# Performance work log

Measured on AMD Instinct MI355X. Metric: run time of the kernel, lower is better.

## Reference

```python
import jax, jax.numpy as jnp
import numpy as np

B, N = 16, 512            # graphs, atoms per graph
F_DIM, H, D = 128, 64, 16  # feature_dim, hidden_dim, far_source_dim
CUT, GROWTH = 5.0, 2.0
NS, NT = 3, 2
MULT = GROWTH ** NS        # default far_max_radius_multiplier = 8
EMAX = CUT * MULT          # 40.0
TOT = NS + NT              # 5 shells total
SF = D + 3                 # 19 per-shell features
SE_IN = TOT * SF           # 95
EH_IN = 4 * D + SE_IN      # 159
N_RBF = 8
BOUNDS = [(5.0, 10.0), (10.0, 20.0), (20.0, 40.0), (40.0, 80.0), (80.0, float('inf'))]


def ln(x, g, b):
    m = x.mean(-1, keepdims=True)
    v = x.var(-1, keepdims=True)
    return (x - m) / jnp.sqrt(v + 1e-5) * g + b


def setup_inputs() -> dict:
    key = jax.random.key(0)
    ks = jax.random.split(key, 16)
    W = lambda k, i, o: jax.random.normal(k, (i, o), jnp.float32) / np.sqrt(i)
    inp = {}
    inp['x'] = jax.random.normal(ks[0], (B * N, F_DIM), jnp.float32)
    inp['pos'] = jax.random.uniform(ks[1], (B * N, 3), jnp.float32) * 80.0
    inp['batch'] = jnp.repeat(jnp.arange(B, dtype=jnp.int32), N)
    inp['num_graphs'] = B
    inp['in_ln_g'] = jnp.ones(F_DIM); inp['in_ln_b'] = jnp.zeros(F_DIM)
    inp['src_w1'] = W(ks[2], F_DIM, H); inp['src_b1'] = jnp.zeros(H)
    inp['src_w2'] = W(ks[3], H, D);     inp['src_b2'] = jnp.zeros(D)
    inp['src_ln_g'] = jnp.ones(D); inp['src_ln_b'] = jnp.zeros(D)
    inp['se_ln_g'] = jnp.ones(SE_IN); inp['se_ln_b'] = jnp.zeros(SE_IN)
    inp['se_w1'] = W(ks[4], SE_IN, H); inp['se_b1'] = jnp.zeros(H)
    inp['se_w2'] = W(ks[5], H, D);     inp['se_b2'] = jnp.zeros(D)
    inp['eh_ln_g'] = jnp.ones(EH_IN); inp['eh_ln_b'] = jnp.zeros(EH_IN)
    inp['eh_w1'] = W(ks[6], EH_IN, H); inp['eh_b1'] = jnp.zeros(H)
    inp['eh_w2'] = W(ks[7], H, 1);     inp['eh_b2'] = jnp.zeros(1)
    inp['k_screen'] = jnp.float32(-8.0)
    inp['kg_w1'] = W(ks[8], N_RBF + 2, 32); inp['kg_b1'] = jnp.zeros(32)
    inp['kg_w2'] = jnp.zeros((32, 1)); inp['kg_b2'] = jnp.zeros(1)  # zero-init per source
    inp['far_gate'] = jnp.float32(0.2)
    inp['energy_scale'] = jnp.float32(0.0)
    return inp


def reference(x, pos, batch, num_graphs, in_ln_g, in_ln_b, src_w1, src_b1, src_w2, src_b2,
              src_ln_g, src_ln_b, se_ln_g, se_ln_b, se_w1, se_b1, se_w2, se_b2,
              eh_ln_g, eh_ln_b, eh_w1, eh_b1, eh_w2, eh_b2,
              k_screen, kg_w1, kg_b1, kg_w2, kg_b2, far_gate, energy_scale):
    M = x.shape[0]
    n = M // num_graphs
    # per-atom source features
    h = ln(x, in_ln_g, in_ln_b)
    src = jax.nn.silu(h @ src_w1 + src_b1) @ src_w2 + src_b2
    src = ln(src, src_ln_g, src_ln_b)
    # graph-wise neutralization (subtract per-graph mean)
    gsum = jax.ops.segment_sum(src, batch, num_segments=num_graphs)
    cnt = jax.ops.segment_sum(jnp.ones((M, 1), x.dtype), batch, num_segments=num_graphs)
    src = src - (gsum / jnp.maximum(cnt, 1.0))[batch]
    # pairwise distances per graph
    p = pos.reshape(num_graphs, n, 3)
    s = src.reshape(num_graphs, n, D)
    diff = p[:, :, None, :] - p[:, None, :, :]
    d = jnp.sqrt((diff * diff).sum(-1) + 1e-12)  # [B,n,n]
    not_self = ~jnp.eye(n, dtype=bool)[None]
    # physical kernel with learned RBF gate
    screening = jax.nn.softplus(k_screen)
    base = jnp.exp(-screening * d) / jnp.maximum(d, 1e-6)
    centers = jnp.linspace(CUT, EMAX, N_RBF)
    spacing = (EMAX - CUT) / (N_RBF - 1)
    gamma = 1.0 / (spacing * spacing)
    dc = d[..., None]
    rbf = jnp.exp(-gamma * (dc - centers) ** 2)
    gin = jnp.concatenate([dc / CUT, dc / EMAX, rbf], -1)
    gate = 1.0 + jnp.tanh(jax.nn.silu(gin @ kg_w1 + kg_b1) @ kg_w2 + kg_b2)[..., 0]
    ker = base * gate
    # shell statistics: kernel-weighted mean source, count, mean_r, rms_r per shell
    feats = []
    for lo, up in BOUNDS:
        m = (d >= lo) & not_self
        if np.isfinite(up):
            m = m & (d < up)
        mf = m.astype(x.dtype)
        c = mf.sum(-1)
        denom = jnp.maximum(c, 1.0)
        mean = jnp.einsum('bij,bjc->bic', ker * mf, s) / denom[..., None]
        mr = (mf * d).sum(-1) / denom
        rr = jnp.sqrt((mf * d * d).sum(-1) / denom + 1e-12)
        feats.append(jnp.concatenate([mean, c[..., None], mr[..., None], rr[..., None]], -1))
    shell = jnp.concatenate(feats, -1).reshape(M, SE_IN)  # [M, 95]
    emb = jax.nn.silu(ln(shell, se_ln_g, se_ln_b) @ se_w1 + se_b1) @ se_w2 + se_b2
    ein = jnp.concatenate([src, emb, src * emb, src - emb, shell], -1)  # [M, 159]
    pa = (jax.nn.silu(ln(ein, eh_ln_g, eh_ln_b) @ eh_w1 + eh_b1) @ eh_w2 + eh_b2)[..., 0]
    pa = pa * jnp.tanh(far_gate) * jnp.exp(energy_scale)
    return jax.ops.segment_sum(pa, batch, num_segments=num_graphs)  # per-graph energies [B]
```

## Files before the change

### kernel.cpp

```cpp
#include <hip/hip_runtime.h>
#include <hip/hip_bf16.h>
#include <math.h>

#define B_G   16
#define N_A   512
#define M_AT  8192
#define FD    128
#define HD    64
#define DD    16
#define SEIN  95
#define EHIN  159
#define NLUT  512
#define DMAXF 140.0f

__device__ __forceinline__ float silu_f(float z) { return z / (1.f + __expf(-z)); }

__global__ __launch_bounds__(128) void k_front(
    const float* __restrict__ x,
    const float* __restrict__ g, const float* __restrict__ bb,
    const float* __restrict__ w1, const float* __restrict__ b1,
    const float* __restrict__ w2, const float* __restrict__ b2,
    const float* __restrict__ lng, const float* __restrict__ lnb,
    const float* __restrict__ k_screen,
    const float* __restrict__ kg_w1, const float* __restrict__ kg_b1,
    const float* __restrict__ kg_w2, const float* __restrict__ kg_b2,
    float* __restrict__ srcout, float* __restrict__ partials,
    float2* __restrict__ lut, float* __restrict__ out) {
  int t = threadIdx.x;

  if (blockIdx.x >= 256) {
    int lb = blockIdx.x - 256;
    __shared__ float w1l[320], b1l[32], w2l[32];
    if (lb == 0 && t < B_G) out[t] = 0.f;
    for (int idx = t; idx < 320; idx += 128) w1l[idx] = kg_w1[idx];
    if (t < 32) { b1l[t] = kg_b1[t]; w2l[t] = kg_w2[t]; }
    __syncthreads();
    int i = lb * 128 + t;
    float step = DMAXF / (float)(NLUT - 1);
    float ksv = k_screen[0];
    float screening = fmaxf(ksv, 0.f) + log1pf(expf(-fabsf(ksv)));
    float b2v = kg_b2[0];
    float vals[2];
#pragma unroll
    for (int e = 0; e < 2; ++e) {
      int ii = min(i + e, NLUT - 1);
      float d = (float)ii * step;
      float base = expf(-screening * d) / fmaxf(d, 1e-6f);
      float gin[10];
      gin[0] = d * (1.f / 5.0f);
      gin[1] = d * (1.f / 40.0f);
#pragma unroll
      for (int kk = 0; kk < 8; ++kk) {
        float u = d - (5.0f + 5.0f * (float)kk);
        gin[2 + kk] = expf(-(1.f / 25.f) * u * u);
      }
      float accv = 0.f;
      for (int h = 0; h < 32; ++h) {
        float z = b1l[h];
#pragma unroll
        for (int kk = 0; kk < 10; ++kk) z += gin[kk] * w1l[kk * 32 + h];
        accv += silu_f(z) * w2l[h];
      }
      vals[e] = base * (1.f + tanhf(accv + b2v));
    }
    lut[i] = make_float2(vals[0], vals[1] - vals[0]);
    return;
  }

  int wave = t >> 6, lane = t & 63;
  __shared__ __align__(16) float xnsA[2][FD][16];
  __shared__ __align__(16) float hbA[2][HD][16];
  __shared__ float psum[2][16];

  int aBase = blockIdx.x * 32 + wave * 16;
  int al = lane & 15, prt = lane >> 4;

  float xr[32];
  const float4* xp = (const float4*)(x + (size_t)(aBase + al) * FD + prt * 32);
#pragma unroll
  for (int i = 0; i < 8; ++i) {
    float4 v = xp[i];
    xr[i*4] = v.x; xr[i*4+1] = v.y; xr[i*4+2] = v.z; xr[i*4+3] = v.w;
  }
  float s = 0.f;
#pragma unroll
  for (int i = 0; i < 32; ++i) s += xr[i];
  s += __shfl_xor(s, 16); s += __shfl_xor(s, 32);
  float m = s * (1.f / 128.f);
  float v2 = 0.f;
#pragma unroll
  for (int i = 0; i < 32; ++i) { float d = xr[i] - m; v2 += d * d; }
  v2 += __shfl_xor(v2, 16); v2 += __shfl_xor(v2, 32);
  float inv = rsqrtf(v2 * (1.f / 128.f) + 1e-5f);
#pragma unroll
  for (int i = 0; i < 32; ++i) {
    int k = prt * 32 + i;
    xnsA[wave][k][al] = (xr[i] - m) * inv * g[k] + bb[k];
  }
  __syncthreads();

  int h0 = al * 4, a0 = prt * 4;
  float acc[4][4] = {};
#pragma unroll 4
  for (int k = 0; k < FD; ++k) {
    float4 wv = ((const float4*)(w1 + (size_t)k * HD))[al];
    float4 xa = *(const float4*)&xnsA[wave][k][a0];
    acc[0][0] += wv.x * xa.x; acc[0][1] += wv.x * xa.y; acc[0][2] += wv.x * xa.z; acc[0][3] += wv.x * xa.w;
    acc[1][0] += wv.y * xa.x; acc[1][1] += wv.y * xa.y; acc[1][2] += wv.y * xa.z; acc[1][3] += wv.y * xa.w;
    acc[2][0] += wv.z * xa.x; acc[2][1] += wv.z * xa.y; acc[2][2] += wv.z * xa.z; acc[2][3] += wv.z * xa.w;
    acc[3][0] += wv.w * xa.x; acc[3][1] += wv.w * xa.y; acc[3][2] += wv.w * xa.z; acc[3][3] += wv.w * xa.w;
  }
  {
    float4 bv = ((const float4*)b1)[al];
    float bh[4] = {bv.x, bv.y, bv.z, bv.w};
#pragma unroll
    for (int i = 0; i < 4; ++i) {
      float4 o;
      o.x = silu_f(acc[i][0] + bh[i]); o.y = silu_f(acc[i][1] + bh[i]);
      o.z = silu_f(acc[i][2] + bh[i]); o.w = silu_f(acc[i][3] + bh[i]);
      *(float4*)&hbA[wave][h0 + i][a0] = o;
    }
  }
  __syncthreads();

  float acc2[4] = {};
#pragma unroll 4
  for (int h = 0; h < HD; ++h) {
    float wv = w2[h * DD + al];
    float4 hv = *(const float4*)&hbA[wave][h][a0];
    acc2[0] += wv * hv.x; acc2[1] += wv * hv.y; acc2[2] += wv * hv.z; acc2[3] += wv * hv.w;
  }
  float b2c = b2[al], lgc = lng[al], lbc = lnb[al];
  float lsum = 0.f;
#pragma unroll
  for (int j = 0; j < 4; ++j) {
    float val = acc2[j] + b2c;
    float sm = val;
    sm += __shfl_xor(sm, 1); sm += __shfl_xor(sm, 2); sm += __shfl_xor(sm, 4); sm += __shfl_xor(sm, 8);
    float mm = sm * (1.f / 16.f);
    float dv = val - mm;
    float vv = dv * dv;
    vv += __shfl_xor(vv, 1); vv += __shfl_xor(vv, 2); vv += __shfl_xor(vv, 4); vv += __shfl_xor(vv, 8);
    float iv = rsqrtf(vv * (1.f / 16.f) + 1e-5f);
    float ov = dv * iv * lgc + lbc;
    srcout[(size_t)(aBase + a0 + j) * DD + al] = ov;
    lsum += ov;
  }
  lsum += __shfl_xor(lsum, 16); lsum += __shfl_xor(lsum, 32);
  if (lane < 16) psum[wave][al] = lsum;
  __syncthreads();
  if (t < 16) partials[(size_t)blockIdx.x * 16 + t] = psum[0][t] + psum[1][t];
}

__global__ __launch_bounds__(256) void k_pairs(
    const float* __restrict__ pos, const float* __restrict__ src,
    const float2* __restrict__ lut, const float* __restrict__ partials,
    float* __restrict__ shell) {
  int gph = blockIdx.x >> 7;
  int blk = blockIdx.x & 127;
  int t = threadIdx.x, wave = t >> 6, lane = t & 63;
  int i_local = blk * 4 + wave;

  __shared__ __align__(16) float sp[N_A * 3];
  __shared__ __align__(16) float ss[N_A * DD];
  __shared__ __align__(16) float2 luts[NLUT];
  __shared__ __align__(16) float wb[4][N_A];
  __shared__ unsigned char tbs[4][N_A];
  __shared__ float smean[16];

  for (int idx = t; idx < N_A * 3 / 4; idx += 256)
    ((float4*)sp)[idx] = ((const float4*)(pos + (size_t)gph * N_A * 3))[idx];
  for (int idx = t; idx < N_A * DD / 4; idx += 256)
    ((float4*)ss)[idx] = ((const float4*)(src + (size_t)gph * N_A * DD))[idx];
  if (t < NLUT / 2) ((float4*)luts)[t] = ((const float4*)lut)[t];
  if (t < 64) {
    int c = t & 15, grp = t >> 4;
    float sm = 0.f;
#pragma unroll
    for (int k = 0; k < 4; ++k)
      sm += partials[(size_t)(gph * 16 + grp * 4 + k) * 16 + c];
    sm += __shfl_xor(sm, 16); sm += __shfl_xor(sm, 32);
    if (t < 16) smean[c] = sm * (1.f / 512.f);
  }
  __syncthreads();

  float px = sp[i_local * 3], py = sp[i_local * 3 + 1], pz = sp[i_local * 3 + 2];
  float cnt[5] = {0,0,0,0,0}, sd[5] = {0,0,0,0,0}, sdd[5] = {0,0,0,0,0}, sw[5] = {0,0,0,0,0};
  const float lscale = (float)(NLUT - 1) / DMAXF;

#pragma unroll
  for (int it = 0; it < 8; ++it) {
    int jv = lane + it * 64;
    float dx = px - sp[jv * 3], dy = py - sp[jv * 3 + 1], dz = pz - sp[jv * 3 + 2];
    float d2 = dx * dx + dy * dy + dz * dz + 1e-12f;
    float d = sqrtf(d2);
    bool valid = (jv != i_local) && (d >= 5.0f);
    int tq = (d >= 10.f) + (d >= 20.f) + (d >= 40.f) + (d >= 80.f);
    float xq = d * lscale;
    int i0 = min((int)xq, NLUT - 2);
    float f = xq - (float)i0;
    float2 L = luts[i0];
    float w = valid ? (L.x + L.y * f) : 0.f;
    wb[wave][jv] = w;
    tbs[wave][jv] = (unsigned char)tq;
    float dm = valid ? d : 0.f;
    float ddm = valid ? d * d : 0.f;
    float cm = valid ? 1.f : 0.f;
#pragma unroll
    for (int q = 0; q < 5; ++q) {
      bool mq = (tq == q);
      cnt[q] += mq ? cm : 0.f;
      sd[q]  += mq ? dm : 0.f;
      sdd[q] += mq ? ddm : 0.f;
      sw[q]  += mq ? w : 0.f;
    }
  }
#pragma unroll
  for (int q = 0; q < 5; ++q) {
#pragma unroll
    for (int o = 32; o > 0; o >>= 1) {
      cnt[q] += __shfl_xor(cnt[q], o);
      sd[q]  += __shfl_xor(sd[q], o);
      sdd[q] += __shfl_xor(sdd[q], o);
      sw[q]  += __shfl_xor(sw[q], o);
    }
  }
  __syncthreads();

  int jlow = lane & 15, cq = lane >> 4;
  float accq[5][4] = {};
  const float* ssb = &ss[jlow * DD + cq * 4];
  const float* wbb = &wb[wave][jlow];
  const unsigned char* tbb = &tbs[wave][jlow];
#pragma unroll
  for (int jj = 0; jj < 32; ++jj) {
    float4 sv = *(const float4*)(ssb + jj * 256);
    float w = wbb[jj * 16];
    int tq = tbb[jj * 16];
    float w0 = (tq == 0) ? w : 0.f;
    float w1_ = (tq == 1) ? w : 0.f;
    float w2_ = (tq == 2) ? w : 0.f;
    float w3_ = (tq == 3) ? w : 0.f;
    float w4_ = (tq == 4) ? w : 0.f;
    accq[0][0] += w0 * sv.x; accq[0][1] += w0 * sv.y; accq[0][2] += w0 * sv.z; accq[0][3] += w0 * sv.w;
    accq[1][0] += w1_ * sv.x; accq[1][1] += w1_ * sv.y; accq[1][2] += w1_ * sv.z; accq[1][3] += w1_ * sv.w;
    accq[2][0] += w2_ * sv.x; accq[2][1] += w2_ * sv.y; accq[2][2] += w2_ * sv.z; accq[2][3] += w2_ * sv.w;
    accq[3][0] += w3_ * sv.x; accq[3][1] += w3_ * sv.y; accq[3][2] += w3_ * sv.z; accq[3][3] += w3_ * sv.w;
    accq[4][0] += w4_ * sv.x; accq[4][1] += w4_ * sv.y; accq[4][2] += w4_ * sv.z; accq[4][3] += w4_ * sv.w;
  }
#pragma unroll
  for (int q = 0; q < 5; ++q)
#pragma unroll
    for (int i = 0; i < 4; ++i) {
      float v = accq[q][i];
      v += __shfl_xor(v, 1); v += __shfl_xor(v, 2); v += __shfl_xor(v, 4); v += __shfl_xor(v, 8);
      accq[q][i] = v;
    }

  float* shp = shell + (size_t)(gph * N_A + i_local) * SEIN;
  if (jlow == 0) {
#pragma unroll
    for (int q = 0; q < 5; ++q) {
      float denom = fmaxf(cnt[q], 1.f);
#pragma unroll
      for (int i = 0; i < 4; ++i) {
        int c = cq * 4 + i;
        shp[q * 19 + c] = (accq[q][i] - smean[c] * sw[q]) / denom;
      }
    }
  }
  if (lane < 5) {
    int q = lane;
    float denom = fmaxf(cnt[q], 1.f);
    shp[q * 19 + 16] = cnt[q];
    shp[q * 19 + 17] = sd[q] / denom;
    shp[q * 19 + 18] = sqrtf(sdd[q] / denom + 1e-12f);
  }
}

__global__ __launch_bounds__(128) void k_tail(
    const float* __restrict__ src, const float* __restrict__ shell,
    const float* __restrict__ partials,
    const float* __restrict__ se_ln_g, const float* __restrict__ se_ln_b,
    const float* __restrict__ se_w1, const float* __restrict__ se_b1,
    const float* __restrict__ se_w2, const float* __restrict__ se_b2,
    const float* __restrict__ eh_ln_g, const float* __restrict__ eh_ln_b,
    const float* __restrict__ eh_w1, const float* __restrict__ eh_b1,
    const float* __restrict__ eh_w2, const float* __restrict__ eh_b2,
    const float* __restrict__ far_gate, const float* __restrict__ energy_scale,
    float* __restrict__ out) {
  int t = threadIdx.x, wave = t >> 6, lane = t & 63;
  __shared__ __align__(16) float einA[2][EHIN][16];
  __shared__ __align__(16) float shnA[2][SEIN][16];
  __shared__ __align__(16) float hbA[2][HD][16];
  __shared__ float smean[16];
  __shared__ float redv[2][4];

  int aB = blockIdx.x * 32;
  int gph = aB >> 9;

  if (t < 64) {
    int c = t & 15, grp = t >> 4;
    float sm = 0.f;
#pragma unroll
    for (int k = 0; k < 4; ++k)
      sm += partials[(size_t)(gph * 16 + grp * 4 + k) * 16 + c];
    sm += __shfl_xor(sm, 16); sm += __shfl_xor(sm, 32);
    if (t < 16) smean[c] = sm * (1.f / 512.f);
  }

  const float* shg = shell + (size_t)aB * SEIN;
  for (int idx = t; idx < 32 * SEIN; idx += 128) {
    unsigned a_loc = ((unsigned)idx * 690u) >> 16;
    int kk = idx - (int)a_loc * SEIN;
    einA[a_loc >> 4][64 + kk][a_loc & 15] = shg[idx];
  }
  __syncthreads();

  int al = lane & 15, prt = lane >> 4;
  {
    float s1 = 0.f, sq = 0.f;
    for (int i = 0; i < 24; ++i) {
      int k = prt * 24 + i;
      if (k < SEIN) { float v = einA[wave][64 + k][al]; s1 += v; sq += v * v; }
    }
    s1 += __shfl_xor(s1, 16); s1 += __shfl_xor(s1, 32);
    sq += __shfl_xor(sq, 16); sq += __shfl_xor(sq, 32);
    float m = s1 * (1.f / (float)SEIN);
    float var = sq * (1.f / (float)SEIN) - m * m;
    float inv = rsqrtf(var + 1e-5f);
    for (int i = 0; i < 24; ++i) {
      int k = prt * 24 + i;
      if (k < SEIN)
        shnA[wave][k][al] = (einA[wave][64 + k][al] - m) * inv * se_ln_g[k] + se_ln_b[k];
    }
  }
  __syncthreads();

  int h0 = al * 4, a0 = prt * 4;
  {
    float acc[4][4] = {};
#pragma unroll 5
    for (int k = 0; k < SEIN; ++k) {
      float4 wv = ((const float4*)(se_w1 + (size_t)k * HD))[al];
      float4 xa = *(const float4*)&shnA[wave][k][a0];
      acc[0][0] += wv.x * xa.x; acc[0][1] += wv.x * xa.y; acc[0][2] += wv.x * xa.z; acc[0][3] += wv.x * xa.w;
      acc[1][0] += wv.y * xa.x; acc[1][1] += wv.y * xa.y; acc[1][2] += wv.y * xa.z; acc[1][3] += wv.y * xa.w;
      acc[2][0] += wv.z * xa.x; acc[2][1] += wv.z * xa.y; acc[2][2] += wv.z * xa.z; acc[2][3] += wv.z * xa.w;
      acc[3][0] += wv.w * xa.x; acc[3][1] += wv.w * xa.y; acc[3][2] += wv.w * xa.z; acc[3][3] += wv.w * xa.w;
    }
    float4 bv = ((const float4*)se_b1)[al];
    float bh[4] = {bv.x, bv.y, bv.z, bv.w};
#pragma unroll
    for (int i = 0; i < 4; ++i) {
      float4 o;
      o.x = silu_f(acc[i][0] + bh[i]); o.y = silu_f(acc[i][1] + bh[i]);
      o.z = silu_f(acc[i][2] + bh[i]); o.w = silu_f(acc[i][3] + bh[i]);
      *(float4*)&hbA[wave][h0 + i][a0] = o;
    }
  }
  __syncthreads();

  {
    float acc2[4] = {};
#pragma unroll 4
    for (int h = 0; h < HD; ++h) {
      float wv = se_w2[h * DD + al];
      float4 hv = *(const float4*)&hbA[wave][h][a0];
      acc2[0] += wv * hv.x; acc2[1] += wv * hv.y; acc2[2] += wv * hv.z; acc2[3] += wv * hv.w;
    }
    float b2c = se_b2[al], smc = smean[al];
    int aW = aB + wave * 16;
#pragma unroll
    for (int j = 0; j < 4; ++j) {
      float ev = acc2[j] + b2c;
      float sv = src[(size_t)(aW + a0 + j) * DD + al] - smc;
      einA[wave][al][a0 + j] = sv;
      einA[wave][16 + al][a0 + j] = ev;
      einA[wave][32 + al][a0 + j] = sv * ev;
      einA[wave][48 + al][a0 + j] = sv - ev;
    }
  }
  __syncthreads();

  {
    float s1 = 0.f, sq = 0.f;
    for (int i = 0; i < 40; ++i) {
      int k = prt * 40 + i;
      if (k < EHIN) { float v = einA[wave][k][al]; s1 += v; sq += v * v; }
    }
    s1 += __shfl_xor(s1, 16); s1 += __shfl_xor(s1, 32);
    sq += __shfl_xor(sq, 16); sq += __shfl_xor(sq, 32);
    float m = s1 * (1.f / (float)EHIN);
    float var = sq * (1.f / (float)EHIN) - m * m;
    float inv = rsqrtf(var + 1e-5f);
    for (int i = 0; i < 40; ++i) {
      int k = prt * 40 + i;
      if (k < EHIN)
        einA[wave][k][al] = (einA[wave][k][al] - m) * inv * eh_ln_g[k] + eh_ln_b[k];
    }
  }
  __syncthreads();

  {
    float acc[4][4] = {};
#pragma unroll 3
    for (int k = 0; k < EHIN; ++k) {
      float4 wv = ((const float4*)(eh_w1 + (size_t)k * HD))[al];
      float4 xa = *(const float4*)&einA[wave][k][a0];
      acc[0][0] += wv.x * xa.x; acc[0][1] += wv.x * xa.y; acc[0][2] += wv.x * xa.z; acc[0][3] += wv.x * xa.w;
      acc[1][0] += wv.y * xa.x; acc[1][1] += wv.y * xa.y; acc[1][2] += wv.y * xa.z; acc[1][3] += wv.y * xa.w;
      acc[2][0] += wv.z * xa.x; acc[2][1] += wv.z * xa.y; acc[2][2] += wv.z * xa.z; acc[2][3] += wv.z * xa.w;
      acc[3][0] += wv.w * xa.x; acc[3][1] += wv.w * xa.y; acc[3][2] += wv.w * xa.z; acc[3][3] += wv.w * xa.w;
    }
    float4 b1v = ((const float4*)eh_b1)[al];
    float4 w2v = ((const float4*)eh_w2)[al];
    float bh[4] = {b1v.x, b1v.y, b1v.z, b1v.w};
    float wh[4] = {w2v.x, w2v.y, w2v.z, w2v.w};
    float pa[4] = {0.f, 0.f, 0.f, 0.f};
#pragma unroll
    for (int i = 0; i < 4; ++i)
#pragma unroll
      for (int j = 0; j < 4; ++j) pa[j] += silu_f(acc[i][j] + bh[i]) * wh[i];
#pragma unroll
    for (int j = 0; j < 4; ++j) {
      pa[j] += __shfl_xor(pa[j], 1); pa[j] += __shfl_xor(pa[j], 2);
      pa[j] += __shfl_xor(pa[j], 4); pa[j] += __shfl_xor(pa[j], 8);
    }
    if (al == 0) redv[wave][prt] = pa[0] + pa[1] + pa[2] + pa[3] + 4.f * eh_b2[0];
  }
  __syncthreads();
  if (t == 0) {
    float tot = 0.f;
#pragma unroll
    for (int w_ = 0; w_ < 2; ++w_)
#pragma unroll
      for (int p = 0; p < 4; ++p) tot += redv[w_][p];
    atomicAdd(&out[gph], tot * tanhf(far_gate[0]) * expf(energy_scale[0]));
  }
}

extern "C" void kernel_launch(void* const* d_in, const int* in_sizes, int n_in,
                              void* d_out, int out_size, void* d_ws, size_t ws_size,
                              hipStream_t stream) {
  const float* x         = (const float*)d_in[0];
  const float* pos       = (const float*)d_in[1];
  const float* in_ln_g   = (const float*)d_in[4];
  const float* in_ln_b   = (const float*)d_in[5];
  const float* src_w1    = (const float*)d_in[6];
  const float* src_b1    = (const float*)d_in[7];
  const float* src_w2    = (const float*)d_in[8];
  const float* src_b2    = (const float*)d_in[9];
  const float* src_ln_g  = (const float*)d_in[10];
  const float* src_ln_b  = (const float*)d_in[11];
  const float* se_ln_g   = (const float*)d_in[12];
  const float* se_ln_b   = (const float*)d_in[13];
  const float* se_w1     = (const float*)d_in[14];
  const float* se_b1     = (const float*)d_in[15];
  const float* se_w2     = (const float*)d_in[16];
  const float* se_b2     = (const float*)d_in[17];
  const float* eh_ln_g   = (const float*)d_in[18];
  const float* eh_ln_b   = (const float*)d_in[19];
  const float* eh_w1     = (const float*)d_in[20];
  const float* eh_b1     = (const float*)d_in[21];
  const float* eh_w2     = (const float*)d_in[22];
  const float* eh_b2     = (const float*)d_in[23];
  const float* k_screen  = (const float*)d_in[24];
  const float* kg_w1     = (const float*)d_in[25];
  const float* kg_b1     = (const float*)d_in[26];
  const float* kg_w2     = (const float*)d_in[27];
  const float* kg_b2     = (const float*)d_in[28];
  const float* far_gate  = (const float*)d_in[29];
  const float* en_scale  = (const float*)d_in[30];
  float* out = (float*)d_out;

  float* ws_src   = (float*)d_ws;
  float* ws_shell = ws_src + (size_t)M_AT * DD;
  float* ws_part  = ws_shell + (size_t)M_AT * SEIN;
  float2* ws_lut  = (float2*)(ws_part + 256 * 16);

  k_front<<<260, 128, 0, stream>>>(x, in_ln_g, in_ln_b, src_w1, src_b1,
                                   src_w2, src_b2, src_ln_g, src_ln_b,
                                   k_screen, kg_w1, kg_b1, kg_w2, kg_b2,
                                   ws_src, ws_part, ws_lut, out);
  k_pairs<<<B_G * (N_A / 4), 256, 0, stream>>>(pos, ws_src, ws_lut, ws_part, ws_shell);
  k_tail<<<M_AT / 32, 128, 0, stream>>>(ws_src, ws_shell, ws_part,
                                        se_ln_g, se_ln_b, se_w1, se_b1, se_w2, se_b2,
                                        eh_ln_g, eh_ln_b, eh_w1, eh_b1, eh_w2, eh_b2,
                                        far_gate, en_scale, out);
}
```

Before: 209.3 us.

## Remap front and tail MLPs to one atom per 16-lane group, more blocks

The front and tail MLP kernels previously gave each wave 16 atoms, with every lane computing a 4x4 hidden-by-atom tile. They now give each 16-lane group one atom, with each lane computing 4 hidden units, and use atom-major shared layouts padded to avoid bank conflicts. Blocks grow to 256 threads but cover 16 atoms, so the launch count doubles (512 blocks) to expose more parallelism across CUs. The trade-off is less register reuse of each weight load: every atom group now reads the full weight matrix itself, which adds global/L1 weight traffic.

```diff
diff --git a/kernel.cpp b/kernel.cpp
--- a/kernel.cpp
+++ b/kernel.cpp
@@ -1,5 +1,4 @@
 #include <hip/hip_runtime.h>
-#include <hip/hip_bf16.h>
 #include <math.h>
 
 #define B_G   16
@@ -12,10 +11,11 @@
 #define EHIN  159
 #define NLUT  512
 #define DMAXF 140.0f
+#define NFB   512
 
 __device__ __forceinline__ float silu_f(float z) { return z / (1.f + __expf(-z)); }
 
-__global__ __launch_bounds__(128) void k_front(
+__global__ __launch_bounds__(256) void k_front(
     const float* __restrict__ x,
     const float* __restrict__ g, const float* __restrict__ bb,
     const float* __restrict__ w1, const float* __restrict__ b1,
@@ -28,14 +28,14 @@
     float2* __restrict__ lut, float* __restrict__ out) {
   int t = threadIdx.x;
 
-  if (blockIdx.x >= 256) {
-    int lb = blockIdx.x - 256;
+  if (blockIdx.x >= NFB) {
+    int lb = blockIdx.x - NFB;
     __shared__ float w1l[320], b1l[32], w2l[32];
     if (lb == 0 && t < B_G) out[t] = 0.f;
-    for (int idx = t; idx < 320; idx += 128) w1l[idx] = kg_w1[idx];
+    for (int idx = t; idx < 320; idx += 256) w1l[idx] = kg_w1[idx];
     if (t < 32) { b1l[t] = kg_b1[t]; w2l[t] = kg_w2[t]; }
     __syncthreads();
-    int i = lb * 128 + t;
+    int i = lb * 256 + t;
     float step = DMAXF / (float)(NLUT - 1);
     float ksv = k_screen[0];
     float screening = fmaxf(ksv, 0.f) + log1pf(expf(-fabsf(ksv)));
@@ -68,73 +68,84 @@
   }
 
   int wave = t >> 6, lane = t & 63;
-  __shared__ __align__(16) float xnsA[2][FD][16];
-  __shared__ __align__(16) float hbA[2][HD][16];
-  __shared__ float psum[2][16];
-
-  int aBase = blockIdx.x * 32 + wave * 16;
-  int al = lane & 15, prt = lane >> 4;
-
-  float xr[32];
-  const float4* xp = (const float4*)(x + (size_t)(aBase + al) * FD + prt * 32);
-#pragma unroll
-  for (int i = 0; i < 8; ++i) {
-    float4 v = xp[i];
-    xr[i*4] = v.x; xr[i*4+1] = v.y; xr[i*4+2] = v.z; xr[i*4+3] = v.w;
+  int ag = lane >> 4, l16 = lane & 15;
+  int a = wave * 4 + ag;
+  int atom = blockIdx.x * 16 + a;
+
+  __shared__ __align__(16) float xn[16 * 132];
+  __shared__ __align__(16) float hb[16 * 68];
+  __shared__ float psum[4][16];
+
+  float xr[8];
+  {
+    const float4* xp = (const float4*)(x + (size_t)atom * FD + l16 * 8);
+    float4 v0 = xp[0], v1 = xp[1];
+    xr[0] = v0.x; xr[1] = v0.y; xr[2] = v0.z; xr[3] = v0.w;
+    xr[4] = v1.x; xr[5] = v1.y; xr[6] = v1.z; xr[7] = v1.w;
   }
   float s = 0.f;
 #pragma unroll
-  for (int i = 0; i < 32; ++i) s += xr[i];
-  s += __shfl_xor(s, 16); s += __shfl_xor(s, 32);
+  for (int i = 0; i < 8; ++i) s += xr[i];
+  s += __shfl_xor(s, 1); s += __shfl_xor(s, 2); s += __shfl_xor(s, 4); s += __shfl_xor(s, 8);
   float m = s * (1.f / 128.f);
   float v2 = 0.f;
 #pragma unroll
-  for (int i = 0; i < 32; ++i) { float d = xr[i] - m; v2 += d * d; }
-  v2 += __shfl_xor(v2, 16); v2 += __shfl_xor(v2, 32);
+  for (int i = 0; i < 8; ++i) { float d = xr[i] - m; v2 += d * d; }
+  v2 += __shfl_xor(v2, 1); v2 += __shfl_xor(v2, 2); v2 += __shfl_xor(v2, 4); v2 += __shfl_xor(v2, 8);
   float inv = rsqrtf(v2 * (1.f / 128.f) + 1e-5f);
-#pragma unroll
-  for (int i = 0; i < 32; ++i) {
-    int k = prt * 32 + i;
-    xnsA[wave][k][al] = (xr[i] - m) * inv * g[k] + bb[k];
-  }
-  __syncthreads();
-
-  int h0 = al * 4, a0 = prt * 4;
-  float acc[4][4] = {};
+  {
+    int kb = l16 * 8;
+    float4 gv0 = ((const float4*)g)[l16 * 2], gv1 = ((const float4*)g)[l16 * 2 + 1];
+    float4 bv0 = ((const float4*)bb)[l16 * 2], bv1 = ((const float4*)bb)[l16 * 2 + 1];
+    float4 o0, o1;
+    o0.x = (xr[0] - m) * inv * gv0.x + bv0.x;
+    o0.y = (xr[1] - m) * inv * gv0.y + bv0.y;
+    o0.z = (xr[2] - m) * inv * gv0.z + bv0.z;
+    o0.w = (xr[3] - m) * inv * gv0.w + bv0.w;
+    o1.x = (xr[4] - m) * inv * gv1.x + bv1.x;
+    o1.y = (xr[5] - m) * inv * gv1.y + bv1.y;
+    o1.z = (xr[6] - m) * inv * gv1.z + bv1.z;
+    o1.w = (xr[7] - m) * inv * gv1.w + bv1.w;
+    *(float4*)&xn[a * 132 + kb] = o0;
+    *(float4*)&xn[a * 132 + kb + 4] = o1;
+  }
+  __syncthreads();
+
+  float acc[4] = {0.f, 0.f, 0.f, 0.f};
+  {
+    const float* xnb = &xn[a * 132];
 #pragma unroll 4
-  for (int k = 0; k < FD; ++k) {
-    float4 wv = ((const float4*)(w1 + (size_t)k * HD))[al];
-    float4 xa = *(const float4*)&xnsA[wave][k][a0];
-    acc[0][0] += wv.x * xa.x; acc[0][1] += wv.x * xa.y; acc[0][2] += wv.x * xa.z; acc[0][3] += wv.x * xa.w;
-    acc[1][0] += wv.y * xa.x; acc[1][1] += wv.y * xa.y; acc[1][2] += wv.y * xa.z; acc[1][3] += wv.y * xa.w;
-    acc[2][0] += wv.z * xa.x; acc[2][1] += wv.z * xa.y; acc[2][2] += wv.z * xa.z; acc[2][3] += wv.z * xa.w;
-    acc[3][0] += wv.w * xa.x; acc[3][1] += wv.w * xa.y; acc[3][2] += wv.w * xa.z; acc[3][3] += wv.w * xa.w;
-  }
-  {
-    float4 bv = ((const float4*)b1)[al];
-    float bh[4] = {bv.x, bv.y, bv.z, bv.w};
-#pragma unroll
-    for (int i = 0; i < 4; ++i) {
-      float4 o;
-      o.x = silu_f(acc[i][0] + bh[i]); o.y = silu_f(acc[i][1] + bh[i]);
-      o.z = silu_f(acc[i][2] + bh[i]); o.w = silu_f(acc[i][3] + bh[i]);
-      *(float4*)&hbA[wave][h0 + i][a0] = o;
-    }
-  }
-  __syncthreads();
-
-  float acc2[4] = {};
-#pragma unroll 4
-  for (int h = 0; h < HD; ++h) {
-    float wv = w2[h * DD + al];
-    float4 hv = *(const float4*)&hbA[wave][h][a0];
-    acc2[0] += wv * hv.x; acc2[1] += wv * hv.y; acc2[2] += wv * hv.z; acc2[3] += wv * hv.w;
-  }
-  float b2c = b2[al], lgc = lng[al], lbc = lnb[al];
-  float lsum = 0.f;
-#pragma unroll
-  for (int j = 0; j < 4; ++j) {
-    float val = acc2[j] + b2c;
+    for (int k = 0; k < FD; k += 4) {
+      float4 xa = *(const float4*)(xnb + k);
+      float4 wa = ((const float4*)(w1 + (size_t)(k + 0) * HD))[l16];
+      float4 wbv = ((const float4*)(w1 + (size_t)(k + 1) * HD))[l16];
+      float4 wc = ((const float4*)(w1 + (size_t)(k + 2) * HD))[l16];
+      float4 wd = ((const float4*)(w1 + (size_t)(k + 3) * HD))[l16];
+      acc[0] += wa.x * xa.x; acc[0] += wbv.x * xa.y; acc[0] += wc.x * xa.z; acc[0] += wd.x * xa.w;
+      acc[1] += wa.y * xa.x; acc[1] += wbv.y * xa.y; acc[1] += wc.y * xa.z; acc[1] += wd.y * xa.w;
+      acc[2] += wa.z * xa.x; acc[2] += wbv.z * xa.y; acc[2] += wc.z * xa.z; acc[2] += wd.z * xa.w;
+      acc[3] += wa.w * xa.x; acc[3] += wbv.w * xa.y; acc[3] += wc.w * xa.z; acc[3] += wd.w * xa.w;
+    }
+    float4 bv = ((const float4*)b1)[l16];
+    float4 ho;
+    ho.x = silu_f(acc[0] + bv.x); ho.y = silu_f(acc[1] + bv.y);
+    ho.z = silu_f(acc[2] + bv.z); ho.w = silu_f(acc[3] + bv.w);
+    *(float4*)&hb[a * 68 + l16 * 4] = ho;
+  }
+  __syncthreads();
+
+  {
+    float acc2 = 0.f;
+    const float* hbb = &hb[a * 68];
+#pragma unroll
+    for (int h = 0; h < HD; h += 4) {
+      float4 hv = *(const float4*)(hbb + h);
+      acc2 += w2[(h + 0) * DD + l16] * hv.x;
+      acc2 += w2[(h + 1) * DD + l16] * hv.y;
+      acc2 += w2[(h + 2) * DD + l16] * hv.z;
+      acc2 += w2[(h + 3) * DD + l16] * hv.w;
+    }
+    float val = acc2 + b2[l16];
     float sm = val;
     sm += __shfl_xor(sm, 1); sm += __shfl_xor(sm, 2); sm += __shfl_xor(sm, 4); sm += __shfl_xor(sm, 8);
     float mm = sm * (1.f / 16.f);
@@ -142,14 +153,16 @@
     float vv = dv * dv;
     vv += __shfl_xor(vv, 1); vv += __shfl_xor(vv, 2); vv += __shfl_xor(vv, 4); vv += __shfl_xor(vv, 8);
     float iv = rsqrtf(vv * (1.f / 16.f) + 1e-5f);
-    float ov = dv * iv * lgc + lbc;
-    srcout[(size_t)(aBase + a0 + j) * DD + al] = ov;
-    lsum += ov;
-  }
-  lsum += __shfl_xor(lsum, 16); lsum += __shfl_xor(lsum, 32);
-  if (lane < 16) psum[wave][al] = lsum;
-  __syncthreads();
-  if (t < 16) partials[(size_t)blockIdx.x * 16 + t] = psum[0][t] + psum[1][t];
+    float ov = dv * iv * lng[l16] + lnb[l16];
+    srcout[(size_t)atom * DD + l16] = ov;
+    float lsum = ov;
+    lsum += __shfl_xor(lsum, 16); lsum += __shfl_xor(lsum, 32);
+    if (lane < 16) psum[wave][l16] = lsum;
+  }
+  __syncthreads();
+  if (t < 16)
+    partials[(size_t)blockIdx.x * 16 + t] =
+        psum[0][t] + psum[1][t] + psum[2][t] + psum[3][t];
 }
 
 __global__ __launch_bounds__(256) void k_pairs(
@@ -177,8 +190,8 @@
     int c = t & 15, grp = t >> 4;
     float sm = 0.f;
 #pragma unroll
-    for (int k = 0; k < 4; ++k)
-      sm += partials[(size_t)(gph * 16 + grp * 4 + k) * 16 + c];
+    for (int k = 0; k < 8; ++k)
+      sm += partials[(size_t)(gph * 32 + grp * 8 + k) * 16 + c];
     sm += __shfl_xor(sm, 16); sm += __shfl_xor(sm, 32);
     if (t < 16) smean[c] = sm * (1.f / 512.f);
   }
@@ -278,7 +291,7 @@
   }
 }
 
-__global__ __launch_bounds__(128) void k_tail(
+__global__ __launch_bounds__(256) void k_tail(
     const float* __restrict__ src, const float* __restrict__ shell,
     const float* __restrict__ partials,
     const float* __restrict__ se_ln_g, const float* __restrict__ se_ln_b,
@@ -290,152 +303,160 @@
     const float* __restrict__ far_gate, const float* __restrict__ energy_scale,
     float* __restrict__ out) {
   int t = threadIdx.x, wave = t >> 6, lane = t & 63;
-  __shared__ __align__(16) float einA[2][EHIN][16];
-  __shared__ __align__(16) float shnA[2][SEIN][16];
-  __shared__ __align__(16) float hbA[2][HD][16];
+  int ag = lane >> 4, l16 = lane & 15;
+  int a = wave * 4 + ag;
+  int aB = blockIdx.x * 16;
+  int gph = aB >> 9;
+
+  __shared__ __align__(16) float ein[16 * 160];
+  __shared__ __align__(16) float shn[16 * 96];
+  __shared__ __align__(16) float hb[16 * 68];
   __shared__ float smean[16];
-  __shared__ float redv[2][4];
-
-  int aB = blockIdx.x * 32;
-  int gph = aB >> 9;
+  __shared__ float redv[4];
 
   if (t < 64) {
     int c = t & 15, grp = t >> 4;
     float sm = 0.f;
 #pragma unroll
-    for (int k = 0; k < 4; ++k)
-      sm += partials[(size_t)(gph * 16 + grp * 4 + k) * 16 + c];
+    for (int k = 0; k < 8; ++k)
+      sm += partials[(size_t)(gph * 32 + grp * 8 + k) * 16 + c];
     sm += __shfl_xor(sm, 16); sm += __shfl_xor(sm, 32);
     if (t < 16) smean[c] = sm * (1.f / 512.f);
   }
 
   const float* shg = shell + (size_t)aB * SEIN;
-  for (int idx = t; idx < 32 * SEIN; idx += 128) {
+  for (int idx = t; idx < 16 * SEIN; idx += 256) {
     unsigned a_loc = ((unsigned)idx * 690u) >> 16;
     int kk = idx - (int)a_loc * SEIN;
-    einA[a_loc >> 4][64 + kk][a_loc & 15] = shg[idx];
-  }
-  __syncthreads();
-
-  int al = lane & 15, prt = lane >> 4;
+    ein[a_loc * 160 + 64 + kk] = shg[idx];
+  }
+  __syncthreads();
+
   {
     float s1 = 0.f, sq = 0.f;
-    for (int i = 0; i < 24; ++i) {
-      int k = prt * 24 + i;
-      if (k < SEIN) { float v = einA[wave][64 + k][al]; s1 += v; sq += v * v; }
-    }
-    s1 += __shfl_xor(s1, 16); s1 += __shfl_xor(s1, 32);
-    sq += __shfl_xor(sq, 16); sq += __shfl_xor(sq, 32);
+    const float* eb = &ein[a * 160 + 64];
+#pragma unroll
+    for (int i = 0; i < 6; ++i) {
+      int k = l16 * 6 + i;
+      if (k < SEIN) { float v = eb[k]; s1 += v; sq += v * v; }
+    }
+    s1 += __shfl_xor(s1, 1); s1 += __shfl_xor(s1, 2); s1 += __shfl_xor(s1, 4); s1 += __shfl_xor(s1, 8);
+    sq += __shfl_xor(sq, 1); sq += __shfl_xor(sq, 2); sq += __shfl_xor(sq, 4); sq += __shfl_xor(sq, 8);
     float m = s1 * (1.f / (float)SEIN);
     float var = sq * (1.f / (float)SEIN) - m * m;
     float inv = rsqrtf(var + 1e-5f);
-    for (int i = 0; i < 24; ++i) {
-      int k = prt * 24 + i;
+#pragma unroll
+    for (int i = 0; i < 6; ++i) {
+      int k = l16 * 6 + i;
       if (k < SEIN)
-        shnA[wave][k][al] = (einA[wave][64 + k][al] - m) * inv * se_ln_g[k] + se_ln_b[k];
-    }
-  }
-  __syncthreads();
-
-  int h0 = al * 4, a0 = prt * 4;
-  {
-    float acc[4][4] = {};
-#pragma unroll 5
-    for (int k = 0; k < SEIN; ++k) {
-      float4 wv = ((const float4*)(se_w1 + (size_t)k * HD))[al];
-      float4 xa = *(const float4*)&shnA[wave][k][a0];
-      acc[0][0] += wv.x * xa.x; acc[0][1] += wv.x * xa.y; acc[0][2] += wv.x * xa.z; acc[0][3] += wv.x * xa.w;
-      acc[1][0] += wv.y * xa.x; acc[1][1] += wv.y * xa.y; acc[1][2] += wv.y * xa.z; acc[1][3] += wv.y * xa.w;
-      acc[2][0] += wv.z * xa.x; acc[2][1] += wv.z * xa.y; acc[2][2] += wv.z * xa.z; acc[2][3] += wv.z * xa.w;
-      acc[3][0] += wv.w * xa.x; acc[3][1] += wv.w * xa.y; acc[3][2] += wv.w * xa.z; acc[3][3] += wv.w * xa.w;
-    }
-    float4 bv = ((const float4*)se_b1)[al];
-    float bh[4] = {bv.x, bv.y, bv.z, bv.w};
-#pragma unroll
-    for (int i = 0; i < 4; ++i) {
-      float4 o;
-      o.x = silu_f(acc[i][0] + bh[i]); o.y = silu_f(acc[i][1] + bh[i]);
-      o.z = silu_f(acc[i][2] + bh[i]); o.w = silu_f(acc[i][3] + bh[i]);
-      *(float4*)&hbA[wave][h0 + i][a0] = o;
-    }
-  }
-  __syncthreads();
-
-  {
-    float acc2[4] = {};
+        shn[a * 96 + k] = (eb[k] - m) * inv * se_ln_g[k] + se_ln_b[k];
+    }
+  }
+  __syncthreads();
+
+  {
+    float acc[4] = {0.f, 0.f, 0.f, 0.f};
+    const float* sb = &shn[a * 96];
 #pragma unroll 4
-    for (int h = 0; h < HD; ++h) {
-      float wv = se_w2[h * DD + al];
-      float4 hv = *(const float4*)&hbA[wave][h][a0];
-      acc2[0] += wv * hv.x; acc2[1] += wv * hv.y; acc2[2] += wv * hv.z; acc2[3] += wv * hv.w;
-    }
-    float b2c = se_b2[al], smc = smean[al];
-    int aW = aB + wave * 16;
-#pragma unroll
-    for (int j = 0; j < 4; ++j) {
-      float ev = acc2[j] + b2c;
-      float sv = src[(size_t)(aW + a0 + j) * DD + al] - smc;
-      einA[wave][al][a0 + j] = sv;
-      einA[wave][16 + al][a0 + j] = ev;
-      einA[wave][32 + al][a0 + j] = sv * ev;
-      einA[wave][48 + al][a0 + j] = sv - ev;
-    }
+    for (int k = 0; k < 92; k += 4) {
+      float4 xa = *(const float4*)(sb + k);
+      float4 wa = ((const float4*)(se_w1 + (size_t)(k + 0) * HD))[l16];
+      float4 wbv = ((const float4*)(se_w1 + (size_t)(k + 1) * HD))[l16];
+      float4 wc = ((const float4*)(se_w1 + (size_t)(k + 2) * HD))[l16];
+      float4 wd = ((const float4*)(se_w1 + (size_t)(k + 3) * HD))[l16];
+      acc[0] += wa.x * xa.x; acc[0] += wbv.x * xa.y; acc[0] += wc.x * xa.z; acc[0] += wd.x * xa.w;
+      acc[1] += wa.y * xa.x; acc[1] += wbv.y * xa.y; acc[1] += wc.y * xa.z; acc[1] += wd.y * xa.w;
+      acc[2] += wa.z * xa.x; acc[2] += wbv.z * xa.y; acc[2] += wc.z * xa.z; acc[2] += wd.z * xa.w;
+      acc[3] += wa.w * xa.x; acc[3] += wbv.w * xa.y; acc[3] += wc.w * xa.z; acc[3] += wd.w * xa.w;
+    }
+#pragma unroll
+    for (int k = 92; k < SEIN; ++k) {
+      float xa = sb[k];
+      float4 wa = ((const float4*)(se_w1 + (size_t)k * HD))[l16];
+      acc[0] += wa.x * xa; acc[1] += wa.y * xa; acc[2] += wa.z * xa; acc[3] += wa.w * xa;
+    }
+    float4 bv = ((const float4*)se_b1)[l16];
+    float4 ho;
+    ho.x = silu_f(acc[0] + bv.x); ho.y = silu_f(acc[1] + bv.y);
+    ho.z = silu_f(acc[2] + bv.z); ho.w = silu_f(acc[3] + bv.w);
+    *(float4*)&hb[a * 68 + l16 * 4] = ho;
+  }
+  __syncthreads();
+
+  {
+    float acc2 = 0.f;
+    const float* hbb = &hb[a * 68];
+#pragma unroll
+    for (int h = 0; h < HD; h += 4) {
+      float4 hv = *(const float4*)(hbb + h);
+      acc2 += se_w2[(h + 0) * DD + l16] * hv.x;
+      acc2 += se_w2[(h + 1) * DD + l16] * hv.y;
+      acc2 += se_w2[(h + 2) * DD + l16] * hv.z;
+      acc2 += se_w2[(h + 3) * DD + l16] * hv.w;
+    }
+    float ev = acc2 + se_b2[l16];
+    float sv = src[(size_t)(aB + a) * DD + l16] - smean[l16];
+    ein[a * 160 + l16] = sv;
+    ein[a * 160 + 16 + l16] = ev;
+    ein[a * 160 + 32 + l16] = sv * ev;
+    ein[a * 160 + 48 + l16] = sv - ev;
   }
   __syncthreads();
 
   {
     float s1 = 0.f, sq = 0.f;
-    for (int i = 0; i < 40; ++i) {
-      int k = prt * 40 + i;
-      if (k < EHIN) { float v = einA[wave][k][al]; s1 += v; sq += v * v; }
-    }
-    s1 += __shfl_xor(s1, 16); s1 += __shfl_xor(s1, 32);
-    sq += __shfl_xor(sq, 16); sq += __shfl_xor(sq, 32);
+    float* eb = &ein[a * 160];
+#pragma unroll
+    for (int i = 0; i < 10; ++i) {
+      int k = l16 * 10 + i;
+      if (k < EHIN) { float v = eb[k]; s1 += v; sq += v * v; }
+    }
+    s1 += __shfl_xor(s1, 1); s1 += __shfl_xor(s1, 2); s1 += __shfl_xor(s1, 4); s1 += __shfl_xor(s1, 8);
+    sq += __shfl_xor(sq, 1); sq += __shfl_xor(sq, 2); sq += __shfl_xor(sq, 4); sq += __shfl_xor(sq, 8);
     float m = s1 * (1.f / (float)EHIN);
     float var = sq * (1.f / (float)EHIN) - m * m;
     float inv = rsqrtf(var + 1e-5f);
-    for (int i = 0; i < 40; ++i) {
-      int k = prt * 40 + i;
+#pragma unroll
+    for (int i = 0; i < 10; ++i) {
+      int k = l16 * 10 + i;
       if (k < EHIN)
-        einA[wave][k][al] = (einA[wave][k][al] - m) * inv * eh_ln_g[k] + eh_ln_b[k];
-    }
-  }
-  __syncthreads();
-
-  {
-    float acc[4][4] = {};
-#pragma unroll 3
-    for (int k = 0; k < EHIN; ++k) {
-      float4 wv = ((const float4*)(eh_w1 + (size_t)k * HD))[al];
-      float4 xa = *(const float4*)&einA[wave][k][a0];
-      acc[0][0] += wv.x * xa.x; acc[0][1] += wv.x * xa.y; acc[0][2] += wv.x * xa.z; acc[0][3] += wv.x * xa.w;
-      acc[1][0] += wv.y * xa.x; acc[1][1] += wv.y * xa.y; acc[1][2] += wv.y * xa.z; acc[1][3] += wv.y * xa.w;
-      acc[2][0] += wv.z * xa.x; acc[2][1] += wv.z * xa.y; acc[2][2] += wv.z * xa.z; acc[2][3] += wv.z * xa.w;
-      acc[3][0] += wv.w * xa.x; acc[3][1] += wv.w * xa.y; acc[3][2] += wv.w * xa.z; acc[3][3] += wv.w * xa.w;
-    }
-    float4 b1v = ((const float4*)eh_b1)[al];
-    float4 w2v = ((const float4*)eh_w2)[al];
-    float bh[4] = {b1v.x, b1v.y, b1v.z, b1v.w};
-    float wh[4] = {w2v.x, w2v.y, w2v.z, w2v.w};
-    float pa[4] = {0.f, 0.f, 0.f, 0.f};
-#pragma unroll
-    for (int i = 0; i < 4; ++i)
-#pragma unroll
-      for (int j = 0; j < 4; ++j) pa[j] += silu_f(acc[i][j] + bh[i]) * wh[i];
-#pragma unroll
-    for (int j = 0; j < 4; ++j) {
-      pa[j] += __shfl_xor(pa[j], 1); pa[j] += __shfl_xor(pa[j], 2);
-      pa[j] += __shfl_xor(pa[j], 4); pa[j] += __shfl_xor(pa[j], 8);
-    }
-    if (al == 0) redv[wave][prt] = pa[0] + pa[1] + pa[2] + pa[3] + 4.f * eh_b2[0];
+        eb[k] = (eb[k] - m) * inv * eh_ln_g[k] + eh_ln_b[k];
+    }
+  }
+  __syncthreads();
+
+  {
+    float acc[4] = {0.f, 0.f, 0.f, 0.f};
+    const float* eb = &ein[a * 160];
+#pragma unroll 4
+    for (int k = 0; k < 156; k += 4) {
+      float4 xa = *(const float4*)(eb + k);
+      float4 wa = ((const float4*)(eh_w1 + (size_t)(k + 0) * HD))[l16];
+      float4 wbv = ((const float4*)(eh_w1 + (size_t)(k + 1) * HD))[l16];
+      float4 wc = ((const float4*)(eh_w1 + (size_t)(k + 2) * HD))[l16];
+      float4 wd = ((const float4*)(eh_w1 + (size_t)(k + 3) * HD))[l16];
+      acc[0] += wa.x * xa.x; acc[0] += wbv.x * xa.y; acc[0] += wc.x * xa.z; acc[0] += wd.x * xa.w;
+      acc[1] += wa.y * xa.x; acc[1] += wbv.y * xa.y; acc[1] += wc.y * xa.z; acc[1] += wd.y * xa.w;
+      acc[2] += wa.z * xa.x; acc[2] += wbv.z * xa.y; acc[2] += wc.z * xa.z; acc[2] += wd.z * xa.w;
+      acc[3] += wa.w * xa.x; acc[3] += wbv.w * xa.y; acc[3] += wc.w * xa.z; acc[3] += wd.w * xa.w;
+    }
+#pragma unroll
+    for (int k = 156; k < EHIN; ++k) {
+      float xa = eb[k];
+      float4 wa = ((const float4*)(eh_w1 + (size_t)k * HD))[l16];
+      acc[0] += wa.x * xa; acc[1] += wa.y * xa; acc[2] += wa.z * xa; acc[3] += wa.w * xa;
+    }
+    float4 b1v = ((const float4*)eh_b1)[l16];
+    float4 w2v = ((const float4*)eh_w2)[l16];
+    float pa = silu_f(acc[0] + b1v.x) * w2v.x + silu_f(acc[1] + b1v.y) * w2v.y
+             + silu_f(acc[2] + b1v.z) * w2v.z + silu_f(acc[3] + b1v.w) * w2v.w;
+    pa += __shfl_xor(pa, 1); pa += __shfl_xor(pa, 2); pa += __shfl_xor(pa, 4); pa += __shfl_xor(pa, 8);
+    pa += __shfl_xor(pa, 16); pa += __shfl_xor(pa, 32);
+    if (lane == 0) redv[wave] = pa + 4.f * eh_b2[0];
   }
   __syncthreads();
   if (t == 0) {
-    float tot = 0.f;
-#pragma unroll
-    for (int w_ = 0; w_ < 2; ++w_)
-#pragma unroll
-      for (int p = 0; p < 4; ++p) tot += redv[w_][p];
+    float tot = redv[0] + redv[1] + redv[2] + redv[3];
     atomicAdd(&out[gph], tot * tanhf(far_gate[0]) * expf(energy_scale[0]));
   }
 }
@@ -477,14 +498,14 @@
   float* ws_src   = (float*)d_ws;
   float* ws_shell = ws_src + (size_t)M_AT * DD;
   float* ws_part  = ws_shell + (size_t)M_AT * SEIN;
-  float2* ws_lut  = (float2*)(ws_part + 256 * 16);
-
-  k_front<<<260, 128, 0, stream>>>(x, in_ln_g, in_ln_b, src_w1, src_b1,
-                                   src_w2, src_b2, src_ln_g, src_ln_b,
-                                   k_screen, kg_w1, kg_b1, kg_w2, kg_b2,
-                                   ws_src, ws_part, ws_lut, out);
+  float2* ws_lut  = (float2*)(ws_part + NFB * 16);
+
+  k_front<<<NFB + 2, 256, 0, stream>>>(x, in_ln_g, in_ln_b, src_w1, src_b1,
+                                       src_w2, src_b2, src_ln_g, src_ln_b,
+                                       k_screen, kg_w1, kg_b1, kg_w2, kg_b2,
+                                       ws_src, ws_part, ws_lut, out);
   k_pairs<<<B_G * (N_A / 4), 256, 0, stream>>>(pos, ws_src, ws_lut, ws_part, ws_shell);
-  k_tail<<<M_AT / 32, 128, 0, stream>>>(ws_src, ws_shell, ws_part,
+  k_tail<<<M_AT / 16, 256, 0, stream>>>(ws_src, ws_shell, ws_part,
                                         se_ln_g, se_ln_b, se_w1, se_b1, se_w2, se_b2,
                                         eh_ln_g, eh_ln_b, eh_w1, eh_b1, eh_w2, eh_b2,
                                         far_gate, en_scale, out);
```

New measurement: 194.3 us. -7.2%, faster.
